# Kernel optimization log

Measured on AMD Instinct MI355X. Metric: run time of the kernel, lower is better.

The kernel has to match this reference:

```python
import jax, jax.numpy as jnp
import numpy as np

B, N, D, H = 8, 1024, 1024, 16
HD = D // H  # head_size = 64


def setup_inputs() -> dict:
    key = jax.random.key(0)
    k0, k1, k2, k3, k4 = jax.random.split(key, 5)
    scale = 1.0 / np.sqrt(D)
    return {
        "x": jax.random.normal(k0, (B, N, D), dtype=jnp.float32),
        "Wqkv": jax.random.normal(k1, (D, 3 * D), dtype=jnp.float32) * scale,
        "bqkv": jnp.zeros((3 * D,), dtype=jnp.float32),
        "Wo": jax.random.normal(k2, (D, D), dtype=jnp.float32) * scale,
        "bo": jnp.zeros((D,), dtype=jnp.float32),
    }


def reference(x, Wqkv, bqkv, Wo, bo):
    # Fused QKV projection: [B, N, 3D]
    qkv = jnp.einsum("bnd,de->bne", x, Wqkv) + bqkv
    q, k, v = jnp.split(qkv, 3, axis=-1)

    def split_heads(t):  # [B, N, D] -> [B, H, N, HD]
        return t.reshape(B, N, H, HD).transpose(0, 2, 1, 3)

    q, k, v = split_heads(q), split_heads(k), split_heads(v)

    # Scaled dot-product attention (no mask, dropout=0)
    scores = jnp.einsum("bhqd,bhkd->bhqk", q, k) / jnp.sqrt(jnp.float32(HD))
    alpha = jax.nn.softmax(scores, axis=-1)
    ctx = jnp.einsum("bhqk,bhkd->bhqd", alpha, v)  # [B, H, N, HD]

    ctx = ctx.transpose(0, 2, 1, 3).reshape(B, N, D)
    out = jnp.einsum("bnd,de->bne", ctx, Wo) + bo
    return out
```

## Files before the change

### kernel.cpp

```cpp
#include <hip/hip_runtime.h>
#include <cstdint>
#include <cstddef>

typedef _Float16 half_t;
typedef __attribute__((ext_vector_type(4))) _Float16 half4v;
typedef __attribute__((ext_vector_type(8))) _Float16 half8v;
typedef __attribute__((ext_vector_type(2))) _Float16 half2v;
typedef __attribute__((ext_vector_type(4))) float float4v;
typedef __attribute__((ext_vector_type(16))) float float16v;
typedef __attribute__((ext_vector_type(4))) unsigned uint4v;
typedef __attribute__((ext_vector_type(2))) int int2v;

typedef __attribute__((address_space(1))) const void gv_t;
typedef __attribute__((address_space(3))) void lv_t;

__device__ __forceinline__ void lds_cp16(const void* g, void* l) {
  __builtin_amdgcn_global_load_lds((gv_t*)g, (lv_t*)l, 16, 0, 0);
}

__device__ __forceinline__ unsigned pkh(float a, float b) {
  return __builtin_bit_cast(unsigned, __builtin_amdgcn_cvt_pkrtz(a, b));
}

__global__ __launch_bounds__(256) void k_cvt(const float* __restrict__ in,
                                             half_t* __restrict__ out) {
  int i = blockIdx.x * 256 + threadIdx.x;
  float4 v = ((const float4*)in)[i];
  half4v h = {(half_t)v.x, (half_t)v.y, (half_t)v.z, (half_t)v.w};
  ((half4v*)out)[i] = h;
}

__global__ __launch_bounds__(256) void k_tcvt(const float* __restrict__ in,
                                              half_t* __restrict__ out, int R, int C) {
  __shared__ float t[32][33];
  int c0 = blockIdx.x * 32, r0 = blockIdx.y * 32;
  int tc = threadIdx.x & 31, tr = threadIdx.x >> 5;
#pragma unroll
  for (int i = 0; i < 4; i++)
    t[tr + i * 8][tc] = in[(size_t)(r0 + tr + i * 8) * C + c0 + tc];
  __syncthreads();
#pragma unroll
  for (int i = 0; i < 4; i++)
    out[(size_t)(c0 + tr + i * 8) * R + r0 + tc] = (half_t)t[tc][tr + i * 8];
}

template <int EPI>
__global__ __launch_bounds__(256) void k_gemm(
    const half_t* __restrict__ A, const half_t* __restrict__ Bt,
    const float* __restrict__ bias, float* __restrict__ Cout,
    half_t* __restrict__ Qo, half_t* __restrict__ Ko, half_t* __restrict__ Vo,
    int M, int N, int K, int NB) {
  __shared__ half_t As[128 * 32];
  __shared__ half_t Bs[128 * 32];
  const int tid = threadIdx.x;
  const int lane = tid & 63;
  const int w = tid >> 6;
  const int nwg = gridDim.x;
  const int cpx = nwg >> 3;
  const int sid = (blockIdx.x & 7) * cpx + (blockIdx.x >> 3);
  const int m0 = (sid / NB) * 128;
  const int n0 = (sid % NB) * 128;
  const int wr = w >> 1, wc = w & 1;

  const int c0 = w * 2, c1 = c0 + 1;
  const int sr0 = c0 * 16 + (lane >> 2);
  const int sr1 = c1 * 16 + (lane >> 2);
  const int scol = (lane & 3) * 8;

  const half_t* Ag0 = A + (size_t)(m0 + sr0) * K + scol;
  const half_t* Ag1 = A + (size_t)(m0 + sr1) * K + scol;
  const half_t* Bg0 = Bt + (size_t)(n0 + sr0) * K + scol;
  const half_t* Bg1 = Bt + (size_t)(n0 + sr1) * K + scol;

  float4v acc[4][4] = {};

  const int fr = lane & 15;
  const int fg = lane >> 4;
  const int aoff = (wr * 64 + fr) * 32 + fg * 8;
  const int boff = (wc * 64 + fr) * 32 + fg * 8;

  for (int kt = 0; kt < K; kt += 32) {
    lds_cp16(Ag0 + kt, As + c0 * 512);
    lds_cp16(Ag1 + kt, As + c1 * 512);
    lds_cp16(Bg0 + kt, Bs + c0 * 512);
    lds_cp16(Bg1 + kt, Bs + c1 * 512);
    __syncthreads();
    half8v a[4], b[4];
#pragma unroll
    for (int m = 0; m < 4; m++) a[m] = *(const half8v*)(As + aoff + m * 512);
#pragma unroll
    for (int n = 0; n < 4; n++) b[n] = *(const half8v*)(Bs + boff + n * 512);
#pragma unroll
    for (int m = 0; m < 4; m++)
#pragma unroll
      for (int n = 0; n < 4; n++)
        acc[m][n] = __builtin_amdgcn_mfma_f32_16x16x32_f16(a[m], b[n], acc[m][n], 0, 0, 0);
    __syncthreads();
  }

  const int rq = (lane >> 4) * 4;
  const int cc = lane & 15;
  if constexpr (EPI == 0) {
#pragma unroll
    for (int n = 0; n < 4; n++) {
      int e = n0 + wc * 64 + n * 16 + cc;
      float bv = bias[e];
      int which = e >> 10, h = (e >> 6) & 15, hd = e & 63;
#pragma unroll
      for (int m = 0; m < 4; m++) {
        int rowb = m0 + wr * 64 + m * 16 + rq;
#pragma unroll
        for (int r = 0; r < 4; r++) {
          int row = rowb + r;
          int b_ = row >> 10, tok = row & 1023;
          half_t hv = (half_t)(acc[m][n][r] + bv);
          size_t bh = (size_t)(b_ * 16 + h);
          if (which == 0)
            Qo[(bh * 1024 + tok) * 64 + hd] = hv;
          else if (which == 1)
            Ko[(bh * 1024 + tok) * 64 + hd] = hv;
          else
            Vo[(bh * 64 + hd) * 1024 + tok] = hv;
        }
      }
    }
  } else {
#pragma unroll
    for (int n = 0; n < 4; n++) {
      int e = n0 + wc * 64 + n * 16 + cc;
      float bv = bias[e];
#pragma unroll
      for (int m = 0; m < 4; m++) {
        int rowb = m0 + wr * 64 + m * 16 + rq;
#pragma unroll
        for (int r = 0; r < 4; r++)
          Cout[(size_t)(rowb + r) * N + e] = acc[m][n][r] + bv;
      }
    }
  }
}

__global__ __launch_bounds__(512, 4) void k_attn(const half_t* __restrict__ Qh,
                                                 const half_t* __restrict__ Kh,
                                                 const half_t* __restrict__ Vt,
                                                 half_t* __restrict__ ctx) {
  __shared__ alignas(16) half_t Ks[2][64 * 64];
  __shared__ alignas(16) half_t Vs[2][64 * 64];
  const int lane = threadIdx.x & 63;
  const int w = threadIdx.x >> 6;
  const int ql = lane & 31, hi = lane >> 5;
  const int xcd = blockIdx.x & 7, loc = blockIdx.x >> 3;
  const int bh = xcd * 16 + (loc >> 2), qb = loc & 3;
  const int b_ = bh >> 4, h = bh & 15;
  const int q0 = qb * 256 + w * 32;

  const half_t* Qp = Qh + (size_t)bh * (1024 * 64);
  const half_t* Kp = Kh + (size_t)bh * (1024 * 64);
  const half_t* Vp = Vt + (size_t)bh * (64 * 1024);

  half8v qf[4];
#pragma unroll
  for (int c = 0; c < 4; c++) {
    half8v tq = *(const half8v*)(Qp + (size_t)(q0 + ql) * 64 + c * 16 + hi * 8);
    qf[c] = tq * (_Float16)0.125f;
  }

  const int G = w * 64 + lane;
  const int rS = G >> 3;
  const int gS = (G & 7) ^ (rS & 7);

  float16v co[2] = {};
  float mr = -1e30f, ssum = 0.f;

  lds_cp16(Kp + (size_t)rS * 64 + gS * 8, &Ks[0][w * 512]);
  lds_cp16(Vp + (size_t)rS * 1024 + 0 + gS * 8, &Vs[0][w * 512]);
  __syncthreads();

  int cur = 0;
  for (int t = 0; t < 16; t++) {
    if (t < 15) {
      const int kn = (t + 1) * 64;
      lds_cp16(Kp + (size_t)(kn + rS) * 64 + gS * 8, &Ks[cur ^ 1][w * 512]);
      lds_cp16(Vp + (size_t)rS * 1024 + kn + gS * 8, &Vs[cur ^ 1][w * 512]);
    }

    float16v sacc[2] = {};
    __builtin_amdgcn_s_setprio(1);
#pragma unroll
    for (int c = 0; c < 4; c++)
#pragma unroll
      for (int s = 0; s < 2; s++) {
        int row = s * 32 + ql;
        half8v kf = *(const half8v*)(&Ks[cur][row * 64 + (((2 * c + hi) ^ (row & 7)) * 8)]);
        sacc[s] = __builtin_amdgcn_mfma_f32_32x32x16_f16(kf, qf[c], sacc[s], 0, 0, 0);
      }
    __builtin_amdgcn_s_setprio(0);

    float mx = -1e30f;
#pragma unroll
    for (int s = 0; s < 2; s++)
#pragma unroll
      for (int i = 0; i < 16; i++) mx = fmaxf(mx, sacc[s][i]);
    mx = fmaxf(mx, __shfl_xor(mx, 32, 64));
    if (mx > mr + 8.f) {
      float fac = __expf(mr - mx);
      mr = mx;
      ssum *= fac;
#pragma unroll
      for (int dd = 0; dd < 2; dd++)
#pragma unroll
        for (int i = 0; i < 16; i++) co[dd][i] *= fac;
    }
    float rsum = 0.f;
#pragma unroll
    for (int s = 0; s < 2; s++)
#pragma unroll
      for (int i = 0; i < 16; i++) {
        float e = __expf(sacc[s][i] - mr);
        sacc[s][i] = e;
        rsum += e;
      }
    rsum += __shfl_xor(rsum, 32, 64);
    ssum += rsum;

#pragma unroll
    for (int kc = 0; kc < 4; kc++) {
      const int s = kc >> 1, o = (kc & 1) * 8;
      unsigned dA0 = pkh(sacc[s][o + 0], sacc[s][o + 1]);
      unsigned dA1 = pkh(sacc[s][o + 2], sacc[s][o + 3]);
      unsigned dB0 = pkh(sacc[s][o + 4], sacc[s][o + 5]);
      unsigned dB1 = pkh(sacc[s][o + 6], sacc[s][o + 7]);
      int2v r0 = __builtin_amdgcn_permlane32_swap((int)dA0, (int)dB0, false, false);
      int2v r1 = __builtin_amdgcn_permlane32_swap((int)dA1, (int)dB1, false, false);
      uint4v pw = {(unsigned)r0.x, (unsigned)r1.x, (unsigned)r0.y, (unsigned)r1.y};
      half8v pf = __builtin_bit_cast(half8v, pw);
      __builtin_amdgcn_s_setprio(1);
#pragma unroll
      for (int dd = 0; dd < 2; dd++) {
        int row = dd * 32 + ql;
        half8v vf = *(const half8v*)(&Vs[cur][row * 64 + (((2 * kc + hi) ^ (row & 7)) * 8)]);
        co[dd] = __builtin_amdgcn_mfma_f32_32x32x16_f16(vf, pf, co[dd], 0, 0, 0);
      }
      __builtin_amdgcn_s_setprio(0);
    }
    __syncthreads();
    cur ^= 1;
  }

  float rinv = 1.0f / ssum;
  half_t* outp = ctx + ((size_t)(b_ * 1024 + q0 + ql) * 1024 + h * 64);
#pragma unroll
  for (int dd = 0; dd < 2; dd++)
#pragma unroll
    for (int g = 0; g < 4; g++) {
      int d0 = dd * 32 + g * 8 + hi * 4;
      unsigned p0 = pkh(co[dd][g * 4 + 0] * rinv, co[dd][g * 4 + 1] * rinv);
      unsigned p1 = pkh(co[dd][g * 4 + 2] * rinv, co[dd][g * 4 + 3] * rinv);
      *(unsigned*)(outp + d0) = p0;
      *(unsigned*)(outp + d0 + 2) = p1;
    }
}

extern "C" void kernel_launch(void* const* d_in, const int* in_sizes, int n_in,
                              void* d_out, int out_size, void* d_ws, size_t ws_size,
                              hipStream_t stream) {
  const float* x = (const float*)d_in[0];
  const float* Wqkv = (const float*)d_in[1];
  const float* bqkv = (const float*)d_in[2];
  const float* Wo = (const float*)d_in[3];
  const float* bo = (const float*)d_in[4];
  float* out = (float*)d_out;
  char* ws = (char*)d_ws;

  const size_t NEED = 75497472;
  if (ws_size < NEED) return;
  half_t* xh = (half_t*)(ws);
  half_t* wqkvT = (half_t*)(ws + 16777216);
  half_t* woT = (half_t*)(ws + 23068672);
  half_t* Qh = (half_t*)(ws + 25165824);
  half_t* Kh = (half_t*)(ws + 41943040);
  half_t* Vt = (half_t*)(ws + 58720256);
  half_t* ctxh = xh;

  k_cvt<<<8192, 256, 0, stream>>>(x, xh);
  k_tcvt<<<dim3(96, 32), 256, 0, stream>>>(Wqkv, wqkvT, 1024, 3072);
  k_tcvt<<<dim3(32, 32), 256, 0, stream>>>(Wo, woT, 1024, 1024);
  k_gemm<0><<<1536, 256, 0, stream>>>(xh, wqkvT, bqkv, nullptr, Qh, Kh, Vt,
                                      8192, 3072, 1024, 24);
  k_attn<<<512, 512, 0, stream>>>(Qh, Kh, Vt, ctxh);
  k_gemm<1><<<512, 256, 0, stream>>>(ctxh, woT, bo, out, nullptr, nullptr, nullptr,
                                     8192, 1024, 1024, 8);
}
```

Before: 207.6 us.

## Double-buffer GEMM LDS tiles, swizzle LDS columns, and remap blocks per XCD

The GEMM kernel now double-buffers its A/B LDS tiles, issuing the next k-tile's global-to-LDS copies before computing on the current one, so each iteration has one barrier instead of two and load latency overlaps with MFMA work. LDS column chunks are XOR-swizzled on both the write and read side to cut bank conflicts on the fragment reads. Block-to-tile mapping is changed so each XCD owns an 8x8 group of tiles, aimed at better L2 reuse. Costs are double the LDS per block, which may lower occupancy, and a mapping hard-coded to these grid sizes.

```diff
diff --git a/kernel.cpp b/kernel.cpp
--- a/kernel.cpp
+++ b/kernel.cpp
@@ -5,7 +5,6 @@
 typedef _Float16 half_t;
 typedef __attribute__((ext_vector_type(4))) _Float16 half4v;
 typedef __attribute__((ext_vector_type(8))) _Float16 half8v;
-typedef __attribute__((ext_vector_type(2))) _Float16 half2v;
 typedef __attribute__((ext_vector_type(4))) float float4v;
 typedef __attribute__((ext_vector_type(16))) float float16v;
 typedef __attribute__((ext_vector_type(4))) unsigned uint4v;
@@ -49,23 +48,24 @@
     const half_t* __restrict__ A, const half_t* __restrict__ Bt,
     const float* __restrict__ bias, float* __restrict__ Cout,
     half_t* __restrict__ Qo, half_t* __restrict__ Ko, half_t* __restrict__ Vo,
-    int M, int N, int K, int NB) {
-  __shared__ half_t As[128 * 32];
-  __shared__ half_t Bs[128 * 32];
+    int M, int N, int K) {
+  __shared__ half_t As[2][128 * 32];
+  __shared__ half_t Bs[2][128 * 32];
   const int tid = threadIdx.x;
   const int lane = tid & 63;
   const int w = tid >> 6;
-  const int nwg = gridDim.x;
-  const int cpx = nwg >> 3;
-  const int sid = (blockIdx.x & 7) * cpx + (blockIdx.x >> 3);
-  const int m0 = (sid / NB) * 128;
-  const int n0 = (sid % NB) * 128;
+  const int xcd = blockIdx.x & 7;
+  const int l = blockIdx.x >> 3;
+  const int nc = l >> 6, r = l & 63;
+  const int m0 = (xcd * 8 + (r >> 3)) * 128;
+  const int n0 = (nc * 8 + (r & 7)) * 128;
   const int wr = w >> 1, wc = w & 1;
 
   const int c0 = w * 2, c1 = c0 + 1;
-  const int sr0 = c0 * 16 + (lane >> 2);
-  const int sr1 = c1 * 16 + (lane >> 2);
-  const int scol = (lane & 3) * 8;
+  const int srow = lane >> 2;
+  const int sr0 = c0 * 16 + srow;
+  const int sr1 = c1 * 16 + srow;
+  const int scol = ((lane & 3) ^ ((lane >> 3) & 3)) * 8;
 
   const half_t* Ag0 = A + (size_t)(m0 + sr0) * K + scol;
   const half_t* Ag1 = A + (size_t)(m0 + sr1) * K + scol;
@@ -76,26 +76,38 @@
 
   const int fr = lane & 15;
   const int fg = lane >> 4;
-  const int aoff = (wr * 64 + fr) * 32 + fg * 8;
-  const int boff = (wc * 64 + fr) * 32 + fg * 8;
-
-  for (int kt = 0; kt < K; kt += 32) {
-    lds_cp16(Ag0 + kt, As + c0 * 512);
-    lds_cp16(Ag1 + kt, As + c1 * 512);
-    lds_cp16(Bg0 + kt, Bs + c0 * 512);
-    lds_cp16(Bg1 + kt, Bs + c1 * 512);
-    __syncthreads();
+  const int cswz = (fg ^ ((fr >> 1) & 3)) * 8;
+  const int aoff = (wr * 64 + fr) * 32 + cswz;
+  const int boff = (wc * 64 + fr) * 32 + cswz;
+
+  lds_cp16(Ag0, &As[0][c0 * 512]);
+  lds_cp16(Ag1, &As[0][c1 * 512]);
+  lds_cp16(Bg0, &Bs[0][c0 * 512]);
+  lds_cp16(Bg1, &Bs[0][c1 * 512]);
+  __syncthreads();
+
+  const int NT = K >> 5;
+  int cur = 0;
+  for (int t = 0; t < NT; t++) {
+    if (t + 1 < NT) {
+      const int kn = (t + 1) * 32;
+      lds_cp16(Ag0 + kn, &As[cur ^ 1][c0 * 512]);
+      lds_cp16(Ag1 + kn, &As[cur ^ 1][c1 * 512]);
+      lds_cp16(Bg0 + kn, &Bs[cur ^ 1][c0 * 512]);
+      lds_cp16(Bg1 + kn, &Bs[cur ^ 1][c1 * 512]);
+    }
     half8v a[4], b[4];
 #pragma unroll
-    for (int m = 0; m < 4; m++) a[m] = *(const half8v*)(As + aoff + m * 512);
-#pragma unroll
-    for (int n = 0; n < 4; n++) b[n] = *(const half8v*)(Bs + boff + n * 512);
+    for (int m = 0; m < 4; m++) a[m] = *(const half8v*)(&As[cur][aoff + m * 512]);
+#pragma unroll
+    for (int n = 0; n < 4; n++) b[n] = *(const half8v*)(&Bs[cur][boff + n * 512]);
 #pragma unroll
     for (int m = 0; m < 4; m++)
 #pragma unroll
       for (int n = 0; n < 4; n++)
         acc[m][n] = __builtin_amdgcn_mfma_f32_16x16x32_f16(a[m], b[n], acc[m][n], 0, 0, 0);
     __syncthreads();
+    cur ^= 1;
   }
 
   const int rq = (lane >> 4) * 4;
@@ -110,10 +122,10 @@
       for (int m = 0; m < 4; m++) {
         int rowb = m0 + wr * 64 + m * 16 + rq;
 #pragma unroll
-        for (int r = 0; r < 4; r++) {
-          int row = rowb + r;
+        for (int r2 = 0; r2 < 4; r2++) {
+          int row = rowb + r2;
           int b_ = row >> 10, tok = row & 1023;
-          half_t hv = (half_t)(acc[m][n][r] + bv);
+          half_t hv = (half_t)(acc[m][n][r2] + bv);
           size_t bh = (size_t)(b_ * 16 + h);
           if (which == 0)
             Qo[(bh * 1024 + tok) * 64 + hd] = hv;
@@ -133,8 +145,8 @@
       for (int m = 0; m < 4; m++) {
         int rowb = m0 + wr * 64 + m * 16 + rq;
 #pragma unroll
-        for (int r = 0; r < 4; r++)
-          Cout[(size_t)(rowb + r) * N + e] = acc[m][n][r] + bv;
+        for (int r2 = 0; r2 < 4; r2++)
+          Cout[(size_t)(rowb + r2) * N + e] = acc[m][n][r2] + bv;
       }
     }
   }
@@ -286,8 +298,8 @@
   k_tcvt<<<dim3(96, 32), 256, 0, stream>>>(Wqkv, wqkvT, 1024, 3072);
   k_tcvt<<<dim3(32, 32), 256, 0, stream>>>(Wo, woT, 1024, 1024);
   k_gemm<0><<<1536, 256, 0, stream>>>(xh, wqkvT, bqkv, nullptr, Qh, Kh, Vt,
-                                      8192, 3072, 1024, 24);
+                                      8192, 3072, 1024);
   k_attn<<<512, 512, 0, stream>>>(Qh, Kh, Vt, ctxh);
   k_gemm<1><<<512, 256, 0, stream>>>(ctxh, woT, bo, out, nullptr, nullptr, nullptr,
-                                     8192, 1024, 1024, 8);
-}
+                                     8192, 1024, 1024);
+}
```

Result: faster. 178.6 us (-14.0%).
